# Kernel tuning notes

Measured on AMD Instinct MI355X. Metric: run time of the kernel, lower is better.

## Reference

```python
import jax, jax.numpy as jnp
import numpy as np

CHANNEL = 256
REDUCTION = 4
GAMMA = 0.5
H_BW = 1.0  # kernel bandwidth h


def setup_inputs() -> dict:
    key = jax.random.key(0)
    k_x, k1, k2, k3, k4 = jax.random.split(key, 5)
    c, r = CHANNEL, CHANNEL // REDUCTION
    x = jax.random.normal(k_x, (32, c, 64, 64), dtype=jnp.float32)
    # fc params, stored as [in, out] for y = x @ W + b (matches nn.Linear math)
    w1 = jax.random.normal(k1, (c, r), dtype=jnp.float32) * (1.0 / np.sqrt(c))
    b1 = jax.random.normal(k2, (r,), dtype=jnp.float32) * 0.01
    w2 = jax.random.normal(k3, (r, c), dtype=jnp.float32) * (1.0 / np.sqrt(r))
    b2 = jax.random.normal(k4, (c,), dtype=jnp.float32) * 0.01
    return {"x": x, "w1": w1, "b1": b1, "w2": w2, "b2": b2}


def reference(x, w1, b1, w2, b2):
    b, c, Hh, Ww = x.shape
    xf = x.reshape(b, c, Hh * Ww)                      # [b, c, n]
    sq = jnp.sum(xf * xf, axis=-1)                     # [b, c]
    gram = jnp.einsum('bcn,bdn->bcd', xf, xf)          # [b, c, c]
    # ||x_i - x_j||^2 = |x_i|^2 + |x_j|^2 - 2 x_i.x_j  (clamped for numerics)
    d2 = jnp.maximum(sq[:, :, None] + sq[:, None, :] - 2.0 * gram, 0.0)
    K = jnp.exp(-0.5 * d2 / (H_BW * H_BW))             # gaussian kernel on dist
    density = jnp.sum(K, axis=-1) / c                  # [b, c]
    hid = jax.nn.relu(density @ w1 + b1)               # [b, c//r]
    attn = jax.nn.sigmoid(hid @ w2 + b2)               # [b, c]
    return x * (attn[:, :, None, None] + GAMMA)
```

## Files before the change

kernel.cpp:

```cpp
#include <hip/hip_runtime.h>
#include <hip/hip_bf16.h>
#include <cstdint>
#include <cstddef>

#define BATCH 32
#define CH    256
#define NSP   4096
#define RED   64
#define GAMMA 0.5f
#define NSPLIT 4
#define KSEG  (NSP / NSPLIT)
#define NKT   (KSEG / 64)
#define TILE_ELEMS (128 * 128)
#define SLICE_STRIDE ((size_t)BATCH * 4 * TILE_ELEMS)

typedef float f32x4 __attribute__((ext_vector_type(4)));
typedef short short8 __attribute__((ext_vector_type(8)));

static __device__ inline unsigned short bfu(float f) {
  __hip_bfloat16 h = __float2bfloat16(f);
  return __builtin_bit_cast(unsigned short, h);
}

__global__ __launch_bounds__(512, 4)
void gram_partial_kernel(const float* __restrict__ x, float* __restrict__ gpart) {
  const int bx   = blockIdx.x;
  const int xcd  = bx & 7;
  const int slot = bx >> 3;
  const int b    = xcd * 4 + (slot >> 4);
  const int rem  = slot & 15;
  const int tile = rem >> 2;
  const int s    = rem & 3;
  const int tr   = tile >> 1;
  const int tc   = tile & 1;
  const int tid  = threadIdx.x;
  const int lane = tid & 63;
  const int wave = tid >> 6;
  const int wr   = wave >> 2;
  const int wc   = wave & 3;

  __shared__ unsigned short lA[128 * 64];
  __shared__ unsigned short lB[128 * 64];

  const int rsub = tid >> 4;
  const int c4   = tid & 15;

  const float* baseA = x + (size_t)(b * CH + tr * 128) * NSP + s * KSEG;
  const float* baseB = x + (size_t)(b * CH + tc * 128) * NSP + s * KSEG;

  f32x4 pa[4], pb[4];
#pragma unroll
  for (int i = 0; i < 4; ++i) {
    int row = i * 32 + rsub;
    pa[i] = *reinterpret_cast<const f32x4*>(baseA + (size_t)row * NSP + c4 * 4);
    pb[i] = *reinterpret_cast<const f32x4*>(baseB + (size_t)row * NSP + c4 * 4);
  }

  f32x4 acc[4][2];
#pragma unroll
  for (int m = 0; m < 4; ++m)
#pragma unroll
    for (int n = 0; n < 2; ++n)
      acc[m][n] = (f32x4){0.f, 0.f, 0.f, 0.f};

  char* cA = (char*)lA;
  char* cB = (char*)lB;

  for (int kt = 0; kt < NKT; ++kt) {
    __syncthreads();
#pragma unroll
    for (int i = 0; i < 4; ++i) {
      int row = i * 32 + rsub;
      int byte = row * 128 + c4 * 8;
      byte ^= (row & 7) << 4;

      uint64_t wa = (uint64_t)bfu(pa[i][0]) | ((uint64_t)bfu(pa[i][1]) << 16) |
                    ((uint64_t)bfu(pa[i][2]) << 32) | ((uint64_t)bfu(pa[i][3]) << 48);
      *reinterpret_cast<uint64_t*>(cA + byte) = wa;

      uint64_t wb = (uint64_t)bfu(pb[i][0]) | ((uint64_t)bfu(pb[i][1]) << 16) |
                    ((uint64_t)bfu(pb[i][2]) << 32) | ((uint64_t)bfu(pb[i][3]) << 48);
      *reinterpret_cast<uint64_t*>(cB + byte) = wb;
    }
    __syncthreads();

    if (kt + 1 < NKT) {
      const float* kA = baseA + (kt + 1) * 64;
      const float* kB = baseB + (kt + 1) * 64;
#pragma unroll
      for (int i = 0; i < 4; ++i) {
        int row = i * 32 + rsub;
        pa[i] = *reinterpret_cast<const f32x4*>(kA + (size_t)row * NSP + c4 * 4);
        pb[i] = *reinterpret_cast<const f32x4*>(kB + (size_t)row * NSP + c4 * 4);
      }
    }

    short8 af[4][2], bff[2][2];
#pragma unroll
    for (int m = 0; m < 4; ++m)
#pragma unroll
      for (int kh = 0; kh < 2; ++kh) {
        int rowa = wr * 64 + m * 16 + (lane & 15);
        int bytea = rowa * 128 + kh * 64 + ((lane >> 4) * 16);
        bytea ^= (rowa & 7) << 4;
        af[m][kh] = *reinterpret_cast<const short8*>(cA + bytea);
      }
#pragma unroll
    for (int n = 0; n < 2; ++n)
#pragma unroll
      for (int kh = 0; kh < 2; ++kh) {
        int rowb = wc * 32 + n * 16 + (lane & 15);
        int byteb = rowb * 128 + kh * 64 + ((lane >> 4) * 16);
        byteb ^= (rowb & 7) << 4;
        bff[n][kh] = *reinterpret_cast<const short8*>(cB + byteb);
      }

#pragma unroll
    for (int m = 0; m < 4; ++m)
#pragma unroll
      for (int n = 0; n < 2; ++n)
#pragma unroll
        for (int kh = 0; kh < 2; ++kh)
          acc[m][n] = __builtin_amdgcn_mfma_f32_16x16x32_bf16(
              af[m][kh], bff[n][kh], acc[m][n], 0, 0, 0);
  }

  float* g = gpart + ((size_t)s * BATCH + b) * 4 * TILE_ELEMS + (size_t)tile * TILE_ELEMS;
#pragma unroll
  for (int m = 0; m < 4; ++m)
#pragma unroll
    for (int n = 0; n < 2; ++n)
#pragma unroll
      for (int r = 0; r < 4; ++r) {
        int row = wr * 64 + m * 16 + ((lane >> 4) * 4 + r);
        int col = wc * 32 + n * 16 + (lane & 15);
        g[row * 128 + col] = acc[m][n][r];
      }
}

__global__ __launch_bounds__(256)
void density_kernel(const float* __restrict__ gpart, float* __restrict__ density) {
  const int blk  = blockIdx.x;
  const int b    = blk >> 3;
  const int rg   = blk & 7;
  const int t    = threadIdx.x;
  const int lane = t & 63;
  const int wave = t >> 6;

  __shared__ float sq[CH];
  {
    int jt = t >> 7, jr = t & 127;
    size_t off = ((size_t)b * 4 + (size_t)jt * 3) * TILE_ELEMS + (size_t)jr * 128 + jr;
    float v = 0.f;
#pragma unroll
    for (int s = 0; s < NSPLIT; ++s) v += gpart[off + (size_t)s * SLICE_STRIDE];
    sq[t] = v;
  }
  __syncthreads();

  const float* gb = gpart + (size_t)b * 4 * TILE_ELEMS;
#pragma unroll 1
  for (int rr = 0; rr < 8; ++rr) {
    int r = rg * 32 + wave * 8 + rr;
    int rt = r >> 7, rrow = r & 127;
    float sqr = sq[r];
    float ssum = 0.f;
#pragma unroll
    for (int cc = 0; cc < 4; ++cc) {
      int j = cc * 64 + lane;
      int jt = j >> 7;
      size_t off = (size_t)(rt * 2 + jt) * TILE_ELEMS + (size_t)rrow * 128 + (j & 127);
      float g = 0.f;
#pragma unroll
      for (int s = 0; s < NSPLIT; ++s) g += gb[off + (size_t)s * SLICE_STRIDE];
      float d2 = fmaxf(sqr + sq[j] - 2.f * g, 0.f);
      ssum += __expf(-0.5f * d2);
    }
    ssum += __shfl_xor(ssum, 1);
    ssum += __shfl_xor(ssum, 2);
    ssum += __shfl_xor(ssum, 4);
    ssum += __shfl_xor(ssum, 8);
    ssum += __shfl_xor(ssum, 16);
    ssum += __shfl_xor(ssum, 32);
    if (lane == 0) density[b * CH + r] = ssum * (1.0f / CH);
  }
}

__global__ __launch_bounds__(256)
void mlp_kernel(const float* __restrict__ density,
                const float* __restrict__ w1, const float* __restrict__ b1,
                const float* __restrict__ w2, const float* __restrict__ b2,
                float* __restrict__ scale) {
  const int b = blockIdx.x;
  const int t = threadIdx.x;
  __shared__ float dens[CH];
  __shared__ float hid[RED];
  dens[t] = density[b * CH + t];
  __syncthreads();
  if (t < RED) {
    float s = b1[t];
#pragma unroll 4
    for (int c = 0; c < CH; ++c) s += dens[c] * w1[c * RED + t];
    hid[t] = fmaxf(s, 0.f);
  }
  __syncthreads();
  float s = b2[t];
#pragma unroll
  for (int h = 0; h < RED; ++h) s += hid[h] * w2[h * CH + t];
  scale[b * CH + t] = 1.f / (1.f + __expf(-s)) + GAMMA;
}

__global__ __launch_bounds__(256)
void scale_kernel(const f32x4* __restrict__ x, const float* __restrict__ scale,
                  f32x4* __restrict__ out, int n4) {
  const int stride = gridDim.x * blockDim.x;
  for (int i = blockIdx.x * blockDim.x + threadIdx.x; i < n4; i += stride) {
    float s = scale[i >> 10];
    __builtin_nontemporal_store(x[i] * s, &out[i]);
  }
}

extern "C" void kernel_launch(void* const* d_in, const int* in_sizes, int n_in,
                              void* d_out, int out_size, void* d_ws, size_t ws_size,
                              hipStream_t stream) {
  const float* x  = (const float*)d_in[0];
  const float* w1 = (const float*)d_in[1];
  const float* b1 = (const float*)d_in[2];
  const float* w2 = (const float*)d_in[3];
  const float* b2 = (const float*)d_in[4];
  float* out = (float*)d_out;

  float* gpart   = (float*)d_ws;
  float* density = gpart + NSPLIT * SLICE_STRIDE;
  float* scale   = density + BATCH * CH;

  gram_partial_kernel<<<dim3(BATCH * 4 * NSPLIT), dim3(512), 0, stream>>>(x, gpart);
  density_kernel<<<dim3(BATCH * 8), dim3(256), 0, stream>>>(gpart, density);
  mlp_kernel<<<dim3(BATCH), dim3(256), 0, stream>>>(density, w1, b1, w2, b2, scale);

  const int n4 = BATCH * CH * NSP / 4;
  scale_kernel<<<dim3(4096), dim3(256), 0, stream>>>(
      (const f32x4*)x, scale, (f32x4*)out, n4);
}
```

Baseline: 107.6 us.

## Store Gram partials in bf16 and share LDS tile on diagonal blocks

Gram partial sums are now written and read as bf16 instead of fp32, halving the workspace traffic between the Gram and density kernels. Diagonal tiles (row tile equals column tile) load and stage only one operand, reusing the A LDS buffer as B and skipping the duplicate global loads and conversions. The bf16 storage of partial Gram values loses precision before d2 = sq_i+sq_j-2g is formed. Because that difference can be small while the terms are large (about 4096), it risks large errors in the kernel density.

```diff
diff --git a/kernel.cpp b/kernel.cpp
--- a/kernel.cpp
+++ b/kernel.cpp
@@ -21,9 +21,13 @@
   __hip_bfloat16 h = __float2bfloat16(f);
   return __builtin_bit_cast(unsigned short, h);
 }
+static __device__ inline float bf2f(unsigned short u) {
+  return __uint_as_float(((uint32_t)u) << 16);
+}
 
 __global__ __launch_bounds__(512, 4)
-void gram_partial_kernel(const float* __restrict__ x, float* __restrict__ gpart) {
+void gram_partial_kernel(const float* __restrict__ x,
+                         unsigned short* __restrict__ gpart) {
   const int bx   = blockIdx.x;
   const int xcd  = bx & 7;
   const int slot = bx >> 3;
@@ -33,6 +37,7 @@
   const int s    = rem & 3;
   const int tr   = tile >> 1;
   const int tc   = tile & 1;
+  const bool diag = (tr == tc);
   const int tid  = threadIdx.x;
   const int lane = tid & 63;
   const int wave = tid >> 6;
@@ -53,7 +58,13 @@
   for (int i = 0; i < 4; ++i) {
     int row = i * 32 + rsub;
     pa[i] = *reinterpret_cast<const f32x4*>(baseA + (size_t)row * NSP + c4 * 4);
-    pb[i] = *reinterpret_cast<const f32x4*>(baseB + (size_t)row * NSP + c4 * 4);
+  }
+  if (!diag) {
+#pragma unroll
+    for (int i = 0; i < 4; ++i) {
+      int row = i * 32 + rsub;
+      pb[i] = *reinterpret_cast<const f32x4*>(baseB + (size_t)row * NSP + c4 * 4);
+    }
   }
 
   f32x4 acc[4][2];
@@ -64,7 +75,7 @@
       acc[m][n] = (f32x4){0.f, 0.f, 0.f, 0.f};
 
   char* cA = (char*)lA;
-  char* cB = (char*)lB;
+  char* cB = diag ? cA : (char*)lB;
 
   for (int kt = 0; kt < NKT; ++kt) {
     __syncthreads();
@@ -78,20 +89,28 @@
                     ((uint64_t)bfu(pa[i][2]) << 32) | ((uint64_t)bfu(pa[i][3]) << 48);
       *reinterpret_cast<uint64_t*>(cA + byte) = wa;
 
-      uint64_t wb = (uint64_t)bfu(pb[i][0]) | ((uint64_t)bfu(pb[i][1]) << 16) |
-                    ((uint64_t)bfu(pb[i][2]) << 32) | ((uint64_t)bfu(pb[i][3]) << 48);
-      *reinterpret_cast<uint64_t*>(cB + byte) = wb;
+      if (!diag) {
+        uint64_t wb = (uint64_t)bfu(pb[i][0]) | ((uint64_t)bfu(pb[i][1]) << 16) |
+                      ((uint64_t)bfu(pb[i][2]) << 32) | ((uint64_t)bfu(pb[i][3]) << 48);
+        *reinterpret_cast<uint64_t*>(cB + byte) = wb;
+      }
     }
     __syncthreads();
 
     if (kt + 1 < NKT) {
       const float* kA = baseA + (kt + 1) * 64;
-      const float* kB = baseB + (kt + 1) * 64;
 #pragma unroll
       for (int i = 0; i < 4; ++i) {
         int row = i * 32 + rsub;
         pa[i] = *reinterpret_cast<const f32x4*>(kA + (size_t)row * NSP + c4 * 4);
-        pb[i] = *reinterpret_cast<const f32x4*>(kB + (size_t)row * NSP + c4 * 4);
+      }
+      if (!diag) {
+        const float* kB = baseB + (kt + 1) * 64;
+#pragma unroll
+        for (int i = 0; i < 4; ++i) {
+          int row = i * 32 + rsub;
+          pb[i] = *reinterpret_cast<const f32x4*>(kB + (size_t)row * NSP + c4 * 4);
+        }
       }
     }
 
@@ -125,7 +144,8 @@
               af[m][kh], bff[n][kh], acc[m][n], 0, 0, 0);
   }
 
-  float* g = gpart + ((size_t)s * BATCH + b) * 4 * TILE_ELEMS + (size_t)tile * TILE_ELEMS;
+  unsigned short* g = gpart + ((size_t)s * BATCH + b) * 4 * TILE_ELEMS
+                            + (size_t)tile * TILE_ELEMS;
 #pragma unroll
   for (int m = 0; m < 4; ++m)
 #pragma unroll
@@ -134,12 +154,13 @@
       for (int r = 0; r < 4; ++r) {
         int row = wr * 64 + m * 16 + ((lane >> 4) * 4 + r);
         int col = wc * 32 + n * 16 + (lane & 15);
-        g[row * 128 + col] = acc[m][n][r];
+        g[row * 128 + col] = bfu(acc[m][n][r]);
       }
 }
 
 __global__ __launch_bounds__(256)
-void density_kernel(const float* __restrict__ gpart, float* __restrict__ density) {
+void density_kernel(const unsigned short* __restrict__ gpart,
+                    float* __restrict__ density) {
   const int blk  = blockIdx.x;
   const int b    = blk >> 3;
   const int rg   = blk & 7;
@@ -150,15 +171,15 @@
   __shared__ float sq[CH];
   {
     int jt = t >> 7, jr = t & 127;
-    size_t off = ((size_t)b * 4 + (size_t)jt * 3) * TILE_ELEMS + (size_t)jr * 128 + jr;
+    size_t off = ((size_t)b * 4 + (size_t)jt * 3) * TILE_ELEMS + (size_t)jr * 129;
     float v = 0.f;
 #pragma unroll
-    for (int s = 0; s < NSPLIT; ++s) v += gpart[off + (size_t)s * SLICE_STRIDE];
+    for (int s = 0; s < NSPLIT; ++s) v += bf2f(gpart[off + (size_t)s * SLICE_STRIDE]);
     sq[t] = v;
   }
   __syncthreads();
 
-  const float* gb = gpart + (size_t)b * 4 * TILE_ELEMS;
+  const unsigned short* gb = gpart + (size_t)b * 4 * TILE_ELEMS;
 #pragma unroll 1
   for (int rr = 0; rr < 8; ++rr) {
     int r = rg * 32 + wave * 8 + rr;
@@ -172,7 +193,7 @@
       size_t off = (size_t)(rt * 2 + jt) * TILE_ELEMS + (size_t)rrow * 128 + (j & 127);
       float g = 0.f;
 #pragma unroll
-      for (int s = 0; s < NSPLIT; ++s) g += gb[off + (size_t)s * SLICE_STRIDE];
+      for (int s = 0; s < NSPLIT; ++s) g += bf2f(gb[off + (size_t)s * SLICE_STRIDE]);
       float d2 = fmaxf(sqr + sq[j] - 2.f * g, 0.f);
       ssum += __expf(-0.5f * d2);
     }
@@ -230,8 +251,8 @@
   const float* b2 = (const float*)d_in[4];
   float* out = (float*)d_out;
 
-  float* gpart   = (float*)d_ws;
-  float* density = gpart + NSPLIT * SLICE_STRIDE;
+  unsigned short* gpart = (unsigned short*)d_ws;
+  float* density = (float*)(gpart + NSPLIT * SLICE_STRIDE);
   float* scale   = density + BATCH * CH;
 
   gram_partial_kernel<<<dim3(BATCH * 4 * NSPLIT), dim3(512), 0, stream>>>(x, gpart);
```

After: 111.1 us. 1.03x slower.

## Compute full 256x256 Gram per block from one shared panel

Applied to the files above, without the earlier changes.

Each block now loads a single 256-row bf16 panel of x into shared memory and computes the whole 256x256 Gram partial with 16 waves, using the same panel for both operands. Before, four 128x128 tiles each loaded separate A and B panels, so x was read four times. The K dimension is now split 8 ways instead of 4. That doubles the partial-sum workspace written by the Gram kernel and read back by the density kernel. The density kernel switches to a contiguous row layout and reads the partial sums with vectorized f32x4 loads.

```diff
diff --git a/kernel.cpp b/kernel.cpp
--- a/kernel.cpp
+++ b/kernel.cpp
@@ -8,11 +8,11 @@
 #define NSP   4096
 #define RED   64
 #define GAMMA 0.5f
-#define NSPLIT 4
+#define NSPLIT 8
 #define KSEG  (NSP / NSPLIT)
 #define NKT   (KSEG / 64)
-#define TILE_ELEMS (128 * 128)
-#define SLICE_STRIDE ((size_t)BATCH * 4 * TILE_ELEMS)
+#define GTILE (CH * CH)
+#define SLICE_STRIDE ((size_t)BATCH * GTILE)
 
 typedef float f32x4 __attribute__((ext_vector_type(4)));
 typedef short short8 __attribute__((ext_vector_type(8)));
@@ -22,119 +22,96 @@
   return __builtin_bit_cast(unsigned short, h);
 }
 
-__global__ __launch_bounds__(512, 4)
-void gram_partial_kernel(const float* __restrict__ x, float* __restrict__ gpart) {
+__global__ __launch_bounds__(1024, 4)
+void gram_sym_kernel(const float* __restrict__ x, float* __restrict__ gpart) {
   const int bx   = blockIdx.x;
-  const int xcd  = bx & 7;
-  const int slot = bx >> 3;
-  const int b    = xcd * 4 + (slot >> 4);
-  const int rem  = slot & 15;
-  const int tile = rem >> 2;
-  const int s    = rem & 3;
-  const int tr   = tile >> 1;
-  const int tc   = tile & 1;
+  const int b    = bx >> 3;
+  const int s    = bx & 7;
   const int tid  = threadIdx.x;
   const int lane = tid & 63;
   const int wave = tid >> 6;
   const int wr   = wave >> 2;
   const int wc   = wave & 3;
 
-  __shared__ unsigned short lA[128 * 64];
-  __shared__ unsigned short lB[128 * 64];
+  __shared__ unsigned short panel[256 * 64];
 
   const int rsub = tid >> 4;
   const int c4   = tid & 15;
 
-  const float* baseA = x + (size_t)(b * CH + tr * 128) * NSP + s * KSEG;
-  const float* baseB = x + (size_t)(b * CH + tc * 128) * NSP + s * KSEG;
-
-  f32x4 pa[4], pb[4];
+  const float* base = x + (size_t)b * CH * NSP + (size_t)s * KSEG;
+
+  f32x4 pa[4];
 #pragma unroll
   for (int i = 0; i < 4; ++i) {
-    int row = i * 32 + rsub;
-    pa[i] = *reinterpret_cast<const f32x4*>(baseA + (size_t)row * NSP + c4 * 4);
-    pb[i] = *reinterpret_cast<const f32x4*>(baseB + (size_t)row * NSP + c4 * 4);
-  }
-
-  f32x4 acc[4][2];
+    int row = i * 64 + rsub;
+    pa[i] = *reinterpret_cast<const f32x4*>(base + (size_t)row * NSP + c4 * 4);
+  }
+
+  f32x4 acc[4][4];
 #pragma unroll
   for (int m = 0; m < 4; ++m)
 #pragma unroll
-    for (int n = 0; n < 2; ++n)
+    for (int n = 0; n < 4; ++n)
       acc[m][n] = (f32x4){0.f, 0.f, 0.f, 0.f};
 
-  char* cA = (char*)lA;
-  char* cB = (char*)lB;
+  char* cP = (char*)panel;
 
   for (int kt = 0; kt < NKT; ++kt) {
     __syncthreads();
 #pragma unroll
     for (int i = 0; i < 4; ++i) {
-      int row = i * 32 + rsub;
+      int row = i * 64 + rsub;
       int byte = row * 128 + c4 * 8;
       byte ^= (row & 7) << 4;
-
-      uint64_t wa = (uint64_t)bfu(pa[i][0]) | ((uint64_t)bfu(pa[i][1]) << 16) |
-                    ((uint64_t)bfu(pa[i][2]) << 32) | ((uint64_t)bfu(pa[i][3]) << 48);
-      *reinterpret_cast<uint64_t*>(cA + byte) = wa;
-
-      uint64_t wb = (uint64_t)bfu(pb[i][0]) | ((uint64_t)bfu(pb[i][1]) << 16) |
-                    ((uint64_t)bfu(pb[i][2]) << 32) | ((uint64_t)bfu(pb[i][3]) << 48);
-      *reinterpret_cast<uint64_t*>(cB + byte) = wb;
+      uint64_t w = (uint64_t)bfu(pa[i][0]) | ((uint64_t)bfu(pa[i][1]) << 16) |
+                   ((uint64_t)bfu(pa[i][2]) << 32) | ((uint64_t)bfu(pa[i][3]) << 48);
+      *reinterpret_cast<uint64_t*>(cP + byte) = w;
     }
     __syncthreads();
 
     if (kt + 1 < NKT) {
-      const float* kA = baseA + (kt + 1) * 64;
-      const float* kB = baseB + (kt + 1) * 64;
+      const float* kB = base + (kt + 1) * 64;
 #pragma unroll
       for (int i = 0; i < 4; ++i) {
-        int row = i * 32 + rsub;
-        pa[i] = *reinterpret_cast<const f32x4*>(kA + (size_t)row * NSP + c4 * 4);
-        pb[i] = *reinterpret_cast<const f32x4*>(kB + (size_t)row * NSP + c4 * 4);
-      }
-    }
-
-    short8 af[4][2], bff[2][2];
-#pragma unroll
-    for (int m = 0; m < 4; ++m)
-#pragma unroll
-      for (int kh = 0; kh < 2; ++kh) {
+        int row = i * 64 + rsub;
+        pa[i] = *reinterpret_cast<const f32x4*>(kB + (size_t)row * NSP + c4 * 4);
+      }
+    }
+
+#pragma unroll
+    for (int kh = 0; kh < 2; ++kh) {
+      short8 af[4];
+#pragma unroll
+      for (int m = 0; m < 4; ++m) {
         int rowa = wr * 64 + m * 16 + (lane & 15);
         int bytea = rowa * 128 + kh * 64 + ((lane >> 4) * 16);
         bytea ^= (rowa & 7) << 4;
-        af[m][kh] = *reinterpret_cast<const short8*>(cA + bytea);
-      }
-#pragma unroll
-    for (int n = 0; n < 2; ++n)
-#pragma unroll
-      for (int kh = 0; kh < 2; ++kh) {
-        int rowb = wc * 32 + n * 16 + (lane & 15);
+        af[m] = *reinterpret_cast<const short8*>(cP + bytea);
+      }
+#pragma unroll
+      for (int n = 0; n < 4; ++n) {
+        int rowb = wc * 64 + n * 16 + (lane & 15);
         int byteb = rowb * 128 + kh * 64 + ((lane >> 4) * 16);
         byteb ^= (rowb & 7) << 4;
-        bff[n][kh] = *reinterpret_cast<const short8*>(cB + byteb);
-      }
-
-#pragma unroll
-    for (int m = 0; m < 4; ++m)
-#pragma unroll
-      for (int n = 0; n < 2; ++n)
-#pragma unroll
-        for (int kh = 0; kh < 2; ++kh)
+        short8 bf = *reinterpret_cast<const short8*>(cP + byteb);
+#pragma unroll
+        for (int m = 0; m < 4; ++m)
           acc[m][n] = __builtin_amdgcn_mfma_f32_16x16x32_bf16(
-              af[m][kh], bff[n][kh], acc[m][n], 0, 0, 0);
-  }
-
-  float* g = gpart + ((size_t)s * BATCH + b) * 4 * TILE_ELEMS + (size_t)tile * TILE_ELEMS;
+              af[m], bf, acc[m][n], 0, 0, 0);
+      }
+    }
+  }
+
+  float* g = gpart + ((size_t)s * BATCH + b) * GTILE;
 #pragma unroll
   for (int m = 0; m < 4; ++m)
 #pragma unroll
-    for (int n = 0; n < 2; ++n)
+    for (int n = 0; n < 4; ++n)
 #pragma unroll
       for (int r = 0; r < 4; ++r) {
         int row = wr * 64 + m * 16 + ((lane >> 4) * 4 + r);
-        int col = wc * 32 + n * 16 + (lane & 15);
-        g[row * 128 + col] = acc[m][n][r];
+        int col = wc * 64 + n * 16 + (lane & 15);
+        g[(size_t)row * CH + col] = acc[m][n][r];
       }
 }
 
@@ -149,8 +126,7 @@
 
   __shared__ float sq[CH];
   {
-    int jt = t >> 7, jr = t & 127;
-    size_t off = ((size_t)b * 4 + (size_t)jt * 3) * TILE_ELEMS + (size_t)jr * 128 + jr;
+    size_t off = (size_t)b * GTILE + (size_t)t * (CH + 1);
     float v = 0.f;
 #pragma unroll
     for (int s = 0; s < NSPLIT; ++s) v += gpart[off + (size_t)s * SLICE_STRIDE];
@@ -158,22 +134,20 @@
   }
   __syncthreads();
 
-  const float* gb = gpart + (size_t)b * 4 * TILE_ELEMS;
+  const float* gb = gpart + (size_t)b * GTILE;
 #pragma unroll 1
   for (int rr = 0; rr < 8; ++rr) {
     int r = rg * 32 + wave * 8 + rr;
-    int rt = r >> 7, rrow = r & 127;
     float sqr = sq[r];
+    size_t off = (size_t)r * CH + lane * 4;
+    f32x4 g = (f32x4){0.f, 0.f, 0.f, 0.f};
+#pragma unroll
+    for (int s = 0; s < NSPLIT; ++s)
+      g += *reinterpret_cast<const f32x4*>(gb + off + (size_t)s * SLICE_STRIDE);
     float ssum = 0.f;
 #pragma unroll
-    for (int cc = 0; cc < 4; ++cc) {
-      int j = cc * 64 + lane;
-      int jt = j >> 7;
-      size_t off = (size_t)(rt * 2 + jt) * TILE_ELEMS + (size_t)rrow * 128 + (j & 127);
-      float g = 0.f;
-#pragma unroll
-      for (int s = 0; s < NSPLIT; ++s) g += gb[off + (size_t)s * SLICE_STRIDE];
-      float d2 = fmaxf(sqr + sq[j] - 2.f * g, 0.f);
+    for (int k = 0; k < 4; ++k) {
+      float d2 = fmaxf(sqr + sq[lane * 4 + k] - 2.f * g[k], 0.f);
       ssum += __expf(-0.5f * d2);
     }
     ssum += __shfl_xor(ssum, 1);
@@ -234,7 +208,7 @@
   float* density = gpart + NSPLIT * SLICE_STRIDE;
   float* scale   = density + BATCH * CH;
 
-  gram_partial_kernel<<<dim3(BATCH * 4 * NSPLIT), dim3(512), 0, stream>>>(x, gpart);
+  gram_sym_kernel<<<dim3(BATCH * NSPLIT), dim3(1024), 0, stream>>>(x, gpart);
   density_kernel<<<dim3(BATCH * 8), dim3(256), 0, stream>>>(gpart, density);
   mlp_kernel<<<dim3(BATCH), dim3(256), 0, stream>>>(density, w1, b1, w2, b2, scale);
 
```

Result: slower. 115.3 us (+7.2%).
